# Kernel optimization log

Hardware: AMD Instinct MI355X
Metric: run time of the kernel (lower is better)

Reference implementation:

```python
import jax, jax.numpy as jnp
import numpy as np

LAMBDA_SOFTMAX = 9.0   # opt.lambda_softmax
LAMBDA_LSE = 6.0       # opt.lambda_lse
MARGIN = 0.2
EPS = 1e-8


def setup_inputs() -> dict:
    key = jax.random.key(0)
    k1, k2, k3, k4 = jax.random.split(key, 4)
    N, F, W, D = 64, 64, 40, 512
    images = jax.random.normal(k1, (N, F, D), dtype=jnp.float32)
    captions = jax.random.normal(k2, (N, W, D), dtype=jnp.float32)
    img_lens = jax.random.randint(k3, (N,), F // 2, F + 1)
    cap_lens = jax.random.randint(k4, (N,), W // 2, W + 1)
    return {"images": images, "captions": captions,
            "img_lens": img_lens, "cap_lens": cap_lens}


def _xattn_scores(images, captions, img_lens, cap_lens):
    # images: (N, F, D) queries; captions: (N, W, D) contexts
    N, F, D = images.shape
    W = captions.shape[1]
    fmask = jnp.arange(F)[None, :] < img_lens[:, None]   # (N_img, F)
    wmask = jnp.arange(W)[None, :] < cap_lens[:, None]   # (N_cap, W)
    # raw attention for every (caption j, image i) pair: (j, i, w, f)
    A = jnp.einsum('jwd,ifd->jiwf', captions, images)
    pair_mask = wmask[:, None, :, None] & fmask[None, :, None, :]
    A = jnp.where(pair_mask, A, 0.0)
    # clipped_l2norm: LeakyReLU(0.1) then l2-normalize along frame axis
    A = jnp.where(A > 0, A, 0.1 * A)
    A = A / (jnp.sqrt(jnp.sum(A * A, axis=3, keepdims=True)) + EPS)
    # softmax over words (sourceL) with temperature lambda_softmax
    logits = jnp.swapaxes(A, 2, 3) * LAMBDA_SOFTMAX       # (j, i, f, w)
    logits = jnp.where(wmask[:, None, None, :], logits, -jnp.inf)
    aw = jax.nn.softmax(logits, axis=-1)                  # (j, i, f, w)
    # weighted context per frame: (j, i, f, d)
    wctx = jnp.einsum('jifw,jwd->jifd', aw, captions)
    # per-frame cosine similarity between image frame and weighted context
    num = jnp.einsum('ifd,jifd->jif', images, wctx)
    n1 = jnp.linalg.norm(images, axis=-1)                 # (i, f)
    n2 = jnp.linalg.norm(wctx, axis=-1)                   # (j, i, f)
    sim = num / jnp.maximum(n1[None, :, :] * n2, EPS)     # (j, i, f)
    # LogSumExp aggregation over valid frames (unstabilized, as in torch)
    e = jnp.exp(sim * LAMBDA_LSE) * fmask[None, :, :]
    scores = jnp.log(jnp.sum(e, axis=-1)) / LAMBDA_LSE    # (n_cap, n_img)
    return scores


def reference(images, captions, img_lens, cap_lens):
    S = _xattn_scores(images, captions, img_lens, cap_lens)  # (N, N)
    diag = jnp.diagonal(S)
    eye = jnp.eye(S.shape[0], dtype=bool)
    cost_s = jnp.maximum(MARGIN + S - diag[:, None], 0.0)
    cost_im = jnp.maximum(MARGIN + S - diag[None, :], 0.0)
    cost_s = jnp.where(eye, 0.0, cost_s)
    cost_im = jnp.where(eye, 0.0, cost_im)
    # max_violation=True: hardest negative per row/col
    return jnp.max(cost_s, axis=1).sum() + jnp.max(cost_im, axis=0).sum()
```

## Files before the change

### kernel.cpp

```cpp
#include <hip/hip_runtime.h>
#include <math.h>

#define N 64
#define F 64
#define W 40
#define D 512
#define LSM 9.0f
#define LLSE 6.0f
#define MARG 0.2f
#define ESTR 56

typedef _Float16 f16x8 __attribute__((ext_vector_type(8)));
typedef _Float16 f16x4 __attribute__((ext_vector_type(4)));
typedef float f32x4 __attribute__((ext_vector_type(4)));

__device__ inline void gll16(const void* g, void* l) {
  __builtin_amdgcn_global_load_lds(
      (const __attribute__((address_space(1))) unsigned int*)g,
      (__attribute__((address_space(3))) unsigned int*)l, 16, 0, 0);
}


__global__ __launch_bounds__(512) void k_pre(
    const float* __restrict__ img, const float* __restrict__ cap,
    _Float16* __restrict__ img_h, _Float16* __restrict__ cap_h,
    _Float16* __restrict__ G_h, float* __restrict__ n1) {
  __shared__ __align__(16) _Float16 capT[4 * 48 * 128];
  int t = threadIdx.x;
  int b = blockIdx.x;
  if (b < 256) {
    int i = b >> 2;
    int f = ((b & 3) << 4) + (t >> 5);
    int q = t & 31;
    const float* row = img + ((size_t)i * F + f) * D + q * 16;
    _Float16* dsti = img_h + (size_t)i * 32768;
    int fsw = (f & 7) << 3;
    float s = 0.f;
    int d0 = q * 16;
    int ch = d0 >> 6, din = d0 & 63;
#pragma unroll
    for (int k = 0; k < 2; ++k) {
      float4 u = *(const float4*)(row + k * 8);
      float4 v = *(const float4*)(row + k * 8 + 4);
      s += u.x * u.x + u.y * u.y + u.z * u.z + u.w * u.w;
      s += v.x * v.x + v.y * v.y + v.z * v.z + v.w * v.w;
      f16x8 h;
      h[0] = (_Float16)u.x; h[1] = (_Float16)u.y; h[2] = (_Float16)u.z; h[3] = (_Float16)u.w;
      h[4] = (_Float16)v.x; h[5] = (_Float16)v.y; h[6] = (_Float16)v.z; h[7] = (_Float16)v.w;
      *(f16x8*)(dsti + ch * 4096 + f * 64 + ((din + k * 8) ^ fsw)) = h;
    }
    s += __shfl_xor(s, 1);
    s += __shfl_xor(s, 2);
    s += __shfl_xor(s, 4);
    s += __shfl_xor(s, 8);
    s += __shfl_xor(s, 16);
    if (q == 0) n1[i * F + f] = sqrtf(s);
  } else {
    int j = b - 256;
    int lane = t & 63, wv = t >> 6;
    const float* src = cap + (size_t)j * W * D;
    _Float16* dst = cap_h + (size_t)j * 24576;
#pragma unroll
    for (int k = 0; k < 6; ++k) {
      int slot = t + k * 512;
      int w = slot >> 6, d = (slot & 63) * 8;
      float4 u = {0.f, 0.f, 0.f, 0.f}, v = {0.f, 0.f, 0.f, 0.f};
      if (w < W) {
        u = *(const float4*)(src + (size_t)w * D + d);
        v = *(const float4*)(src + (size_t)w * D + d + 4);
      }
      f16x8 h;
      h[0] = (_Float16)u.x; h[1] = (_Float16)u.y; h[2] = (_Float16)u.z; h[3] = (_Float16)u.w;
      h[4] = (_Float16)v.x; h[5] = (_Float16)v.y; h[6] = (_Float16)v.z; h[7] = (_Float16)v.w;
      int wsw = (w & 7) << 3;
      int ch2 = d >> 6, din2 = d & 63;
      *(f16x8*)(dst + ch2 * 3072 + w * 64 + (din2 ^ wsw)) = h;
      int chO = d >> 7, dinO = d & 127;
      *(f16x8*)(capT + chO * 6144 + w * 128 + (dinO ^ wsw)) = h;
    }
    __syncthreads();
    int rlo = lane & 15, hi = lane >> 4;
    int koff = hi * 8, sw = (rlo & 7) << 3;
    _Float16* gb = G_h + (size_t)j * 3072;
    for (int tile = wv; tile < 9; tile += 8) {
      int mt = tile / 3, kt = tile % 3;
      f32x4 acc = (f32x4)0.f;
#pragma unroll
      for (int ks = 0; ks < 16; ++ks) {
        int kk = ks * 32 + koff;
        int ch = kk >> 7, din = (kk & 127) ^ sw;
        f16x8 af = *(const f16x8*)(capT + ch * 6144 + (mt * 16 + rlo) * 128 + din);
        f16x8 bf = *(const f16x8*)(capT + ch * 6144 + (kt * 16 + rlo) * 128 + din);
        acc = __builtin_amdgcn_mfma_f32_16x16x32_f16(af, bf, acc, 0, 0, 0);
      }
#pragma unroll
      for (int r = 0; r < 4; ++r) {
        int w = mt * 16 + hi * 4 + r, k = kt * 16 + rlo;
        float val = (w < W && k < W) ? acc[r] : 0.f;
        gb[w * 64 + k] = (_Float16)val;
      }
    }
    if (t < 96) {
      int w = t >> 1, c8 = 48 + (t & 1) * 8;
      *(f16x8*)(gb + w * 64 + c8) = (f16x8)(_Float16)0.f;
    }
  }
}

__global__ __launch_bounds__(512, 4) void k_main(
    const _Float16* __restrict__ img_h, const _Float16* __restrict__ cap_h,
    const int* __restrict__ imgL, const int* __restrict__ capL,
    const float* __restrict__ n1g, const _Float16* __restrict__ G_h,
    float* __restrict__ S) {
  __shared__ __align__(16) char buf[81920];

  int t = threadIdx.x;
  int lane = t & 63, wv = t >> 6;
  int rlo = lane & 15, hi = lane >> 4;
  int koff = hi * 8;
  int sw = (rlo & 7) << 3;

  int bid = blockIdx.x;
  int xcd = bid & 7, s0 = bid >> 3;
  int jloc = wv & 3, iloc = wv >> 2;
  int i = (xcd & 3) * 16 + (s0 & 7) * 2 + iloc;
  int j = (xcd >> 2) * 32 + (s0 >> 3) * 4 + jloc;

  int iL = imgL[i], cL = capL[j];

  const char* capb = (const char*)cap_h + (size_t)(j - jloc) * 49152;
  const char* imgb = (const char*)img_h + (size_t)(i - iloc) * 65536;

  const char* bsrc[5];
  int cstr[5], mdst[5];
#pragma unroll
  for (int s = 0; s < 5; ++s) {
    int m = s * 8 + wv;
    if (m < 24) {
      bsrc[s] = capb + (m / 6) * 49152 + (m % 6) * 1024 + lane * 16;
      cstr[s] = 6144;
    } else {
      int e = m - 24;
      bsrc[s] = imgb + (e >> 3) * 65536 + (e & 7) * 1024 + lane * 16;
      cstr[s] = 8192;
    }
    mdst[s] = m * 1024;
  }

  f32x4 acc[3][4];
#pragma unroll
  for (int mt = 0; mt < 3; ++mt)
#pragma unroll
    for (int nt = 0; nt < 4; ++nt) acc[mt][nt] = (f32x4)0.f;

#pragma unroll
  for (int s = 0; s < 5; ++s) gll16(bsrc[s], buf + mdst[s]);

#pragma unroll
  for (int c = 0; c < 8; ++c) {
    if (c < 7) {
      char* db = buf + ((c + 1) & 1) * 40960;
#pragma unroll
      for (int s = 0; s < 5; ++s) gll16(bsrc[s] + (c + 1) * cstr[s], db + mdst[s]);
      asm volatile("s_waitcnt vmcnt(5)" ::: "memory");
    } else {
      asm volatile("s_waitcnt vmcnt(0)" ::: "memory");
    }
    __builtin_amdgcn_s_barrier();
    __builtin_amdgcn_sched_barrier(0);
    const char* cb = buf + (c & 1) * 40960;
    const _Float16* myCap = (const _Float16*)cb + jloc * 3072;
    const _Float16* myImg = (const _Float16*)(cb + 24576) + iloc * 4096;
#pragma unroll
    for (int ks = 0; ks < 2; ++ks) {
      int col = (ks * 32 + koff) ^ sw;
      f16x8 af[3], bf[4];
#pragma unroll
      for (int mt = 0; mt < 3; ++mt) af[mt] = *(const f16x8*)(myCap + (mt * 16 + rlo) * 64 + col);
#pragma unroll
      for (int nt = 0; nt < 4; ++nt) bf[nt] = *(const f16x8*)(myImg + (nt * 16 + rlo) * 64 + col);
#pragma unroll
      for (int mt = 0; mt < 3; ++mt)
#pragma unroll
        for (int nt = 0; nt < 4; ++nt)
          acc[mt][nt] = __builtin_amdgcn_mfma_f32_16x16x32_f16(af[mt], bf[nt], acc[mt][nt], 0, 0, 0);
    }
    __builtin_amdgcn_sched_barrier(0);
    __builtin_amdgcn_s_barrier();
  }

  _Float16* Ew = (_Float16*)(buf + wv * 7168);
  float n1lane = n1g[i * F + lane];

  float rinv[3][4];
#pragma unroll
  for (int mt = 0; mt < 3; ++mt)
#pragma unroll
    for (int r = 0; r < 4; ++r) {
      float s = 0.f;
#pragma unroll
      for (int nt = 0; nt < 4; ++nt) {
        float a = acc[mt][nt][r];
        float l = a > 0.f ? a : 0.1f * a;
        s += ((nt * 16 + rlo) < iL) ? l * l : 0.f;
      }
#pragma unroll
      for (int d = 1; d < 16; d <<= 1) s += __shfl_xor(s, d);
      rinv[mt][r] = 1.f / (sqrtf(s) + 1e-8f);
    }

  float sn[4] = {0.f, 0.f, 0.f, 0.f};
#pragma unroll
  for (int mt = 0; mt < 3; ++mt)
#pragma unroll
    for (int nt = 0; nt < 4; ++nt) {
      f16x4 ev;
#pragma unroll
      for (int r = 0; r < 4; ++r) {
        int w = mt * 16 + hi * 4 + r;
        float a = acc[mt][nt][r];
        float l = a > 0.f ? a : 0.1f * a;
        float e = (w < cL) ? __expf(LSM * l * rinv[mt][r]) : 0.f;
        sn[nt] = fmaf(e, a, sn[nt]);
        ev[r] = (_Float16)e;
      }
      *(f16x4*)(Ew + (nt * 16 + rlo) * ESTR + mt * 16 + hi * 4) = ev;
    }
#pragma unroll
  for (int nt = 0; nt < 4; ++nt) {
    sn[nt] += __shfl_xor(sn[nt], 16);
    sn[nt] += __shfl_xor(sn[nt], 32);
  }

  const _Float16* gB = G_h + (size_t)j * 3072 + rlo * 64 + koff;
  f32x4 P[4][3];
#pragma unroll
  for (int mtl = 0; mtl < 4; ++mtl)
#pragma unroll
    for (int ntl = 0; ntl < 3; ++ntl) P[mtl][ntl] = (f32x4)0.f;
#pragma unroll
  for (int ks2 = 0; ks2 < 2; ++ks2) {
    int kk2 = ks2 * 32;
    f16x8 bfg[3];
#pragma unroll
    for (int ntl = 0; ntl < 3; ++ntl) bfg[ntl] = *(const f16x8*)(gB + ntl * 1024 + kk2);
#pragma unroll
    for (int mtl = 0; mtl < 4; ++mtl) {
      f16x8 af = *(const f16x8*)(Ew + (mtl * 16 + rlo) * ESTR + kk2 + koff);
#pragma unroll
      for (int ntl = 0; ntl < 3; ++ntl)
        P[mtl][ntl] = __builtin_amdgcn_mfma_f32_16x16x32_f16(af, bfg[ntl], P[mtl][ntl], 0, 0, 0);
    }
  }

  float ef = 0.f;
#pragma unroll
  for (int mtl = 0; mtl < 4; ++mtl) {
#pragma unroll
    for (int rr = 0; rr < 4; ++rr) {
      int fm = mtl * 16 + hi * 4 + rr;
      float n2s = 0.f;
#pragma unroll
      for (int ntl = 0; ntl < 3; ++ntl) {
        float evv = (float)Ew[fm * ESTR + ntl * 16 + rlo];
        n2s = fmaf(P[mtl][ntl][rr], evv, n2s);
      }
#pragma unroll
      for (int d = 1; d < 16; d <<= 1) n2s += __shfl_xor(n2s, d);
      float nm = __shfl(sn[mtl], hi * 4 + rr);
      float n1v = __shfl(n1lane, fm);
      float denom = n1v * sqrtf(fmaxf(n2s, 0.f));
      float sim = nm / fmaxf(denom, 1e-20f);
      ef += (fm < iL) ? __expf(LLSE * sim) : 0.f;
    }
  }
  ef += __shfl_xor(ef, 16);
  ef += __shfl_xor(ef, 32);
  if (lane == 0) S[(j << 6) + i] = __logf(ef) * (1.f / LLSE);
}

__global__ void k_loss(const float* __restrict__ S, float* __restrict__ out) {
  __shared__ float red[128];
  int t = threadIdx.x;
  float m = -1e30f;
  if (t < 64) {
    int a = t;
    float da = S[a * N + a];
    for (int b = 0; b < N; ++b)
      if (b != a) m = fmaxf(m, MARG + S[a * N + b] - da);
  } else {
    int b = t - 64;
    float db = S[b * N + b];
    for (int a = 0; a < N; ++a)
      if (a != b) m = fmaxf(m, MARG + S[a * N + b] - db);
  }
  red[t] = fmaxf(m, 0.f);
  __syncthreads();
  if (t < 64) {
    float v = red[t] + red[t + 64];
#pragma unroll
    for (int off = 1; off < 64; off <<= 1) v += __shfl_xor(v, off);
    if (t == 0) *out = v;
  }
}

extern "C" void kernel_launch(void* const* d_in, const int* in_sizes, int n_in,
                              void* d_out, int out_size, void* d_ws, size_t ws_size,
                              hipStream_t stream) {
  const float* img = (const float*)d_in[0];
  const float* cap = (const float*)d_in[1];
  const int* imgL = (const int*)d_in[2];
  const int* capL = (const int*)d_in[3];

  char* wsb = (char*)d_ws;
  float* n1 = (float*)wsb;
  float* S = (float*)(wsb + 16384);
  _Float16* img_h = (_Float16*)(wsb + 32768);
  _Float16* cap_h = (_Float16*)(wsb + 32768 + 4194304);
  _Float16* G_h = (_Float16*)(wsb + 32768 + 4194304 + 3145728);

  k_pre<<<320, 512, 0, stream>>>(img, cap, img_h, cap_h, G_h, n1);
  k_main<<<512, 512, 0, stream>>>(img_h, cap_h, imgL, capL, n1, G_h, S);
  k_loss<<<1, 128, 0, stream>>>(S, (float*)d_out);
}
```

Baseline: 56.74 us.

## Split fused attention kernel into GEMM kernel and separate epilogue kernel

The fused main kernel is split in two. k_gemm computes the raw caption-image attention tiles, applies the masks, and writes them to global memory as fp16. A new k_epi kernel, one 256-thread block per pair, reloads each tile and does the LeakyReLU norm, softmax, G-based context norm and LSE in shared memory. This is meant to ease register pressure and raise parallelism in the epilogue, at the cost of an extra kernel launch and a roughly 20 MB global round trip for the attention tiles.

```diff
diff --git a/kernel.cpp b/kernel.cpp
--- a/kernel.cpp
+++ b/kernel.cpp
@@ -8,7 +8,6 @@
 #define LSM 9.0f
 #define LLSE 6.0f
 #define MARG 0.2f
-#define ESTR 56
 
 typedef _Float16 f16x8 __attribute__((ext_vector_type(8)));
 typedef _Float16 f16x4 __attribute__((ext_vector_type(4)));
@@ -79,7 +78,8 @@
       *(f16x8*)(capT + chO * 6144 + w * 128 + (dinO ^ wsw)) = h;
     }
     __syncthreads();
-    int rlo = lane & 15, hi = lane >> 4;
+    int lane2 = t & 63;
+    int rlo = lane2 & 15, hi = lane2 >> 4;
     int koff = hi * 8, sw = (rlo & 7) << 3;
     _Float16* gb = G_h + (size_t)j * 3072;
     for (int tile = wv; tile < 9; tile += 8) {
@@ -107,11 +107,10 @@
   }
 }
 
-__global__ __launch_bounds__(512, 4) void k_main(
+__global__ __launch_bounds__(512, 4) void k_gemm(
     const _Float16* __restrict__ img_h, const _Float16* __restrict__ cap_h,
     const int* __restrict__ imgL, const int* __restrict__ capL,
-    const float* __restrict__ n1g, const _Float16* __restrict__ G_h,
-    float* __restrict__ S) {
+    _Float16* __restrict__ A_g) {
   __shared__ __align__(16) char buf[81920];
 
   int t = threadIdx.x;
@@ -189,94 +188,132 @@
     __builtin_amdgcn_s_barrier();
   }
 
-  _Float16* Ew = (_Float16*)(buf + wv * 7168);
-  float n1lane = n1g[i * F + lane];
-
-  float rinv[3][4];
+  _Float16* Ag = A_g + (size_t)((j << 6) + i) * 2560;
 #pragma unroll
   for (int mt = 0; mt < 3; ++mt)
 #pragma unroll
     for (int r = 0; r < 4; ++r) {
-      float s = 0.f;
-#pragma unroll
-      for (int nt = 0; nt < 4; ++nt) {
-        float a = acc[mt][nt][r];
+      int w = mt * 16 + hi * 4 + r;
+      if (w < W) {
+#pragma unroll
+        for (int nt = 0; nt < 4; ++nt) {
+          int f = nt * 16 + rlo;
+          float v = (w < cL && f < iL) ? acc[mt][nt][r] : 0.f;
+          Ag[w * 64 + f] = (_Float16)v;
+        }
+      }
+    }
+}
+
+__global__ __launch_bounds__(256, 8) void k_epi(
+    const _Float16* __restrict__ A_g, const _Float16* __restrict__ G_h,
+    const int* __restrict__ imgL, const int* __restrict__ capL,
+    const float* __restrict__ n1g, float* __restrict__ S) {
+  __shared__ __align__(16) _Float16 Al[40 * 72];
+  __shared__ __align__(16) _Float16 Es[64 * 72];
+  __shared__ float rinv_s[W];
+  __shared__ float numu[F];
+  __shared__ float red[4];
+
+  int t = threadIdx.x;
+  int lane = t & 63, wv = t >> 6;
+  int rlo = lane & 15, hi = lane >> 4;
+  int koff = hi * 8;
+
+  int bid = blockIdx.x;
+  int j = bid >> 6, i = bid & 63;
+  int iL = imgL[i], cL = capL[j];
+
+  for (int k = t; k < 576; k += 256) ((f16x8*)Es)[k] = (f16x8)(_Float16)0.f;
+
+  if (t < 160) {
+    const _Float16* src = A_g + (size_t)bid * 2560 + t * 16;
+    f16x8 a0 = *(const f16x8*)src;
+    f16x8 a1 = *(const f16x8*)(src + 8);
+    int row = t >> 2, colb = (t & 3) * 16;
+    *(f16x8*)(Al + row * 72 + colb) = a0;
+    *(f16x8*)(Al + row * 72 + colb + 8) = a1;
+  }
+  __syncthreads();
+
+  if (t < 160) {
+    int w = t >> 2, q = t & 3;
+    const _Float16* p = Al + w * 72 + q * 16;
+    float s = 0.f;
+#pragma unroll
+    for (int k = 0; k < 2; ++k) {
+      f16x8 h = *(const f16x8*)(p + k * 8);
+#pragma unroll
+      for (int e = 0; e < 8; ++e) {
+        float a = (float)h[e];
         float l = a > 0.f ? a : 0.1f * a;
-        s += ((nt * 16 + rlo) < iL) ? l * l : 0.f;
-      }
-#pragma unroll
-      for (int d = 1; d < 16; d <<= 1) s += __shfl_xor(s, d);
-      rinv[mt][r] = 1.f / (sqrtf(s) + 1e-8f);
-    }
-
-  float sn[4] = {0.f, 0.f, 0.f, 0.f};
-#pragma unroll
-  for (int mt = 0; mt < 3; ++mt)
-#pragma unroll
-    for (int nt = 0; nt < 4; ++nt) {
-      f16x4 ev;
-#pragma unroll
-      for (int r = 0; r < 4; ++r) {
-        int w = mt * 16 + hi * 4 + r;
-        float a = acc[mt][nt][r];
-        float l = a > 0.f ? a : 0.1f * a;
-        float e = (w < cL) ? __expf(LSM * l * rinv[mt][r]) : 0.f;
-        sn[nt] = fmaf(e, a, sn[nt]);
-        ev[r] = (_Float16)e;
-      }
-      *(f16x4*)(Ew + (nt * 16 + rlo) * ESTR + mt * 16 + hi * 4) = ev;
-    }
-#pragma unroll
-  for (int nt = 0; nt < 4; ++nt) {
-    sn[nt] += __shfl_xor(sn[nt], 16);
-    sn[nt] += __shfl_xor(sn[nt], 32);
-  }
-
-  const _Float16* gB = G_h + (size_t)j * 3072 + rlo * 64 + koff;
-  f32x4 P[4][3];
-#pragma unroll
-  for (int mtl = 0; mtl < 4; ++mtl)
-#pragma unroll
-    for (int ntl = 0; ntl < 3; ++ntl) P[mtl][ntl] = (f32x4)0.f;
+        s += l * l;
+      }
+    }
+    s += __shfl_xor(s, 1);
+    s += __shfl_xor(s, 2);
+    if (q == 0) rinv_s[w] = 1.f / (sqrtf(s) + 1e-8f);
+  }
+  __syncthreads();
+
+  {
+    int c = t & 3, f = t >> 2;
+    float sn = 0.f;
+#pragma unroll
+    for (int k = 0; k < 10; ++k) {
+      int w = c + 4 * k;
+      float a = (float)Al[w * 72 + f];
+      float l = a > 0.f ? a : 0.1f * a;
+      float e = (w < cL) ? __expf(LSM * l * rinv_s[w]) : 0.f;
+      sn = fmaf(e, a, sn);
+      Es[f * 72 + w] = (_Float16)e;
+    }
+    sn += __shfl_xor(sn, 1);
+    sn += __shfl_xor(sn, 2);
+    if (c == 0) numu[f] = sn;
+  }
+  __syncthreads();
+
+  int fr = wv * 16 + rlo;
+  const _Float16* gB = G_h + (size_t)j * 3072;
+  f32x4 P[3];
+#pragma unroll
+  for (int ntl = 0; ntl < 3; ++ntl) P[ntl] = (f32x4)0.f;
 #pragma unroll
   for (int ks2 = 0; ks2 < 2; ++ks2) {
-    int kk2 = ks2 * 32;
-    f16x8 bfg[3];
-#pragma unroll
-    for (int ntl = 0; ntl < 3; ++ntl) bfg[ntl] = *(const f16x8*)(gB + ntl * 1024 + kk2);
-#pragma unroll
-    for (int mtl = 0; mtl < 4; ++mtl) {
-      f16x8 af = *(const f16x8*)(Ew + (mtl * 16 + rlo) * ESTR + kk2 + koff);
-#pragma unroll
-      for (int ntl = 0; ntl < 3; ++ntl)
-        P[mtl][ntl] = __builtin_amdgcn_mfma_f32_16x16x32_f16(af, bfg[ntl], P[mtl][ntl], 0, 0, 0);
+    int kk = ks2 * 32 + koff;
+    f16x8 ea = *(const f16x8*)(Es + fr * 72 + kk);
+#pragma unroll
+    for (int ntl = 0; ntl < 3; ++ntl) {
+      f16x8 gb = *(const f16x8*)(gB + (ntl * 16 + rlo) * 64 + kk);
+      P[ntl] = __builtin_amdgcn_mfma_f32_16x16x32_f16(ea, gb, P[ntl], 0, 0, 0);
     }
   }
 
   float ef = 0.f;
 #pragma unroll
-  for (int mtl = 0; mtl < 4; ++mtl) {
-#pragma unroll
-    for (int rr = 0; rr < 4; ++rr) {
-      int fm = mtl * 16 + hi * 4 + rr;
-      float n2s = 0.f;
-#pragma unroll
-      for (int ntl = 0; ntl < 3; ++ntl) {
-        float evv = (float)Ew[fm * ESTR + ntl * 16 + rlo];
-        n2s = fmaf(P[mtl][ntl][rr], evv, n2s);
-      }
-#pragma unroll
-      for (int d = 1; d < 16; d <<= 1) n2s += __shfl_xor(n2s, d);
-      float nm = __shfl(sn[mtl], hi * 4 + rr);
-      float n1v = __shfl(n1lane, fm);
-      float denom = n1v * sqrtf(fmaxf(n2s, 0.f));
-      float sim = nm / fmaxf(denom, 1e-20f);
-      ef += (fm < iL) ? __expf(LLSE * sim) : 0.f;
-    }
-  }
-  ef += __shfl_xor(ef, 16);
-  ef += __shfl_xor(ef, 32);
-  if (lane == 0) S[(j << 6) + i] = __logf(ef) * (1.f / LLSE);
+  for (int rr = 0; rr < 4; ++rr) {
+    int fm = wv * 16 + hi * 4 + rr;
+    float n2s = 0.f;
+#pragma unroll
+    for (int ntl = 0; ntl < 3; ++ntl) {
+      float evv = (float)Es[fm * 72 + ntl * 16 + rlo];
+      n2s = fmaf(P[ntl][rr], evv, n2s);
+    }
+#pragma unroll
+    for (int d = 1; d < 16; d <<= 1) n2s += __shfl_xor(n2s, d);
+    float nm = numu[fm];
+    float n1v = n1g[i * F + fm];
+    float denom = n1v * sqrtf(fmaxf(n2s, 0.f));
+    float sim = nm / fmaxf(denom, 1e-20f);
+    ef += (fm < iL) ? __expf(LLSE * sim) : 0.f;
+  }
+  float val = (rlo == 0) ? ef : 0.f;
+#pragma unroll
+  for (int d = 1; d < 64; d <<= 1) val += __shfl_xor(val, d);
+  if (lane == 0) red[wv] = val;
+  __syncthreads();
+  if (t == 0) S[(j << 6) + i] = __logf(red[0] + red[1] + red[2] + red[3]) * (1.f / LLSE);
 }
 
 __global__ void k_loss(const float* __restrict__ S, float* __restrict__ out) {
@@ -318,8 +355,10 @@
   _Float16* img_h = (_Float16*)(wsb + 32768);
   _Float16* cap_h = (_Float16*)(wsb + 32768 + 4194304);
   _Float16* G_h = (_Float16*)(wsb + 32768 + 4194304 + 3145728);
+  _Float16* A_g = (_Float16*)(wsb + 32768 + 4194304 + 3145728 + 393216);
 
   k_pre<<<320, 512, 0, stream>>>(img, cap, img_h, cap_h, G_h, n1);
-  k_main<<<512, 512, 0, stream>>>(img_h, cap_h, imgL, capL, n1, G_h, S);
+  k_gemm<<<512, 512, 0, stream>>>(img_h, cap_h, imgL, capL, A_g);
+  k_epi<<<4096, 256, 0, stream>>>(A_g, G_h, imgL, capL, n1, S);
   k_loss<<<1, 128, 0, stream>>>(S, (float*)d_out);
 }
```

Measured after the change: 61.70 us. +8.8%, slower.

## Enlarge main-kernel block tile to 4 captions by 4 images with 2 pairs per wave

Applied to the files above, without the earlier changes.

The block tile grows from 4 captions x 2 images to 4 captions x 4 images, so the grid drops from 512 to 256 blocks and each fp16 chunk staged in LDS is reused by twice as many waves. Each wave now accumulates a 6x4 MFMA tile covering two caption-image pairs, then runs the softmax, context-norm and LSE epilogue twice in sequence. MFMA sections are wrapped in s_setprio to raise wave priority. The trade-off is a larger LDS buffer (112 KB), fewer resident blocks, more accumulator registers per wave and a longer serial epilogue per wave, which leaves less parallelism to hide latency.

```diff
diff --git a/kernel.cpp b/kernel.cpp
--- a/kernel.cpp
+++ b/kernel.cpp
@@ -79,7 +79,8 @@
       *(f16x8*)(capT + chO * 6144 + w * 128 + (dinO ^ wsw)) = h;
     }
     __syncthreads();
-    int rlo = lane & 15, hi = lane >> 4;
+    int lane2 = t & 63;
+    int rlo = lane2 & 15, hi = lane2 >> 4;
     int koff = hi * 8, sw = (rlo & 7) << 3;
     _Float16* gb = G_h + (size_t)j * 3072;
     for (int tile = wv; tile < 9; tile += 8) {
@@ -107,34 +108,37 @@
   }
 }
 
-__global__ __launch_bounds__(512, 4) void k_main(
+__global__ __launch_bounds__(512, 2) void k_fused(
     const _Float16* __restrict__ img_h, const _Float16* __restrict__ cap_h,
     const int* __restrict__ imgL, const int* __restrict__ capL,
     const float* __restrict__ n1g, const _Float16* __restrict__ G_h,
     float* __restrict__ S) {
-  __shared__ __align__(16) char buf[81920];
+  __shared__ __align__(16) char buf[114688];
 
   int t = threadIdx.x;
   int lane = t & 63, wv = t >> 6;
   int rlo = lane & 15, hi = lane >> 4;
   int koff = hi * 8;
   int sw = (rlo & 7) << 3;
+  int wm = wv >> 2, wn = wv & 3;
 
   int bid = blockIdx.x;
   int xcd = bid & 7, s0 = bid >> 3;
-  int jloc = wv & 3, iloc = wv >> 2;
-  int i = (xcd & 3) * 16 + (s0 & 7) * 2 + iloc;
-  int j = (xcd >> 2) * 32 + (s0 >> 3) * 4 + jloc;
-
-  int iL = imgL[i], cL = capL[j];
-
-  const char* capb = (const char*)cap_h + (size_t)(j - jloc) * 49152;
-  const char* imgb = (const char*)img_h + (size_t)(i - iloc) * 65536;
-
-  const char* bsrc[5];
-  int cstr[5], mdst[5];
-#pragma unroll
-  for (int s = 0; s < 5; ++s) {
+  int bj = (xcd & 3) * 4 + (s0 & 3);
+  int bi = (xcd >> 2) * 8 + (s0 >> 2);
+
+  int i = bi * 4 + wn;
+  int ja = bj * 4 + wm * 2;
+  int iL = imgL[i];
+  int cLa = capL[ja], cLb = capL[ja + 1];
+
+  const char* capb = (const char*)cap_h + (size_t)bj * 4 * 49152;
+  const char* imgb = (const char*)img_h + (size_t)bi * 4 * 65536;
+
+  const char* bsrc[7];
+  int cstr[7], mdst[7];
+#pragma unroll
+  for (int s = 0; s < 7; ++s) {
     int m = s * 8 + wv;
     if (m < 24) {
       bsrc[s] = capb + (m / 6) * 49152 + (m % 6) * 1024 + lane * 16;
@@ -147,43 +151,49 @@
     mdst[s] = m * 1024;
   }
 
-  f32x4 acc[3][4];
-#pragma unroll
-  for (int mt = 0; mt < 3; ++mt)
+  f32x4 acc[6][4];
+#pragma unroll
+  for (int mt = 0; mt < 6; ++mt)
 #pragma unroll
     for (int nt = 0; nt < 4; ++nt) acc[mt][nt] = (f32x4)0.f;
 
 #pragma unroll
-  for (int s = 0; s < 5; ++s) gll16(bsrc[s], buf + mdst[s]);
+  for (int s = 0; s < 7; ++s) gll16(bsrc[s], buf + mdst[s]);
 
 #pragma unroll
   for (int c = 0; c < 8; ++c) {
     if (c < 7) {
-      char* db = buf + ((c + 1) & 1) * 40960;
-#pragma unroll
-      for (int s = 0; s < 5; ++s) gll16(bsrc[s] + (c + 1) * cstr[s], db + mdst[s]);
-      asm volatile("s_waitcnt vmcnt(5)" ::: "memory");
+      char* db = buf + ((c + 1) & 1) * 57344;
+#pragma unroll
+      for (int s = 0; s < 7; ++s) gll16(bsrc[s] + (c + 1) * cstr[s], db + mdst[s]);
+      asm volatile("s_waitcnt vmcnt(7)" ::: "memory");
     } else {
       asm volatile("s_waitcnt vmcnt(0)" ::: "memory");
     }
     __builtin_amdgcn_s_barrier();
     __builtin_amdgcn_sched_barrier(0);
-    const char* cb = buf + (c & 1) * 40960;
-    const _Float16* myCap = (const _Float16*)cb + jloc * 3072;
-    const _Float16* myImg = (const _Float16*)(cb + 24576) + iloc * 4096;
+    const char* cb = buf + (c & 1) * 57344;
+    const _Float16* Al = (const _Float16*)cb;
+    const _Float16* Bl = (const _Float16*)(cb + 24576) + wn * 4096;
 #pragma unroll
     for (int ks = 0; ks < 2; ++ks) {
       int col = (ks * 32 + koff) ^ sw;
-      f16x8 af[3], bf[4];
-#pragma unroll
-      for (int mt = 0; mt < 3; ++mt) af[mt] = *(const f16x8*)(myCap + (mt * 16 + rlo) * 64 + col);
-#pragma unroll
-      for (int nt = 0; nt < 4; ++nt) bf[nt] = *(const f16x8*)(myImg + (nt * 16 + rlo) * 64 + col);
-#pragma unroll
-      for (int mt = 0; mt < 3; ++mt)
+      f16x8 bf[4], af[6];
+#pragma unroll
+      for (int nt = 0; nt < 4; ++nt) bf[nt] = *(const f16x8*)(Bl + (nt * 16 + rlo) * 64 + col);
+#pragma unroll
+      for (int mt = 0; mt < 6; ++mt) {
+        int blk = wm * 2 + (mt >= 3 ? 1 : 0);
+        int w = (mt >= 3 ? mt - 3 : mt) * 16 + rlo;
+        af[mt] = *(const f16x8*)(Al + blk * 3072 + w * 64 + col);
+      }
+      __builtin_amdgcn_s_setprio(1);
+#pragma unroll
+      for (int mt = 0; mt < 6; ++mt)
 #pragma unroll
         for (int nt = 0; nt < 4; ++nt)
           acc[mt][nt] = __builtin_amdgcn_mfma_f32_16x16x32_f16(af[mt], bf[nt], acc[mt][nt], 0, 0, 0);
+      __builtin_amdgcn_s_setprio(0);
     }
     __builtin_amdgcn_sched_barrier(0);
     __builtin_amdgcn_s_barrier();
@@ -192,91 +202,98 @@
   _Float16* Ew = (_Float16*)(buf + wv * 7168);
   float n1lane = n1g[i * F + lane];
 
-  float rinv[3][4];
-#pragma unroll
-  for (int mt = 0; mt < 3; ++mt)
-#pragma unroll
-    for (int r = 0; r < 4; ++r) {
-      float s = 0.f;
+#pragma unroll
+  for (int p = 0; p < 2; ++p) {
+    int j = ja + p;
+    int cL = p ? cLb : cLa;
+    int mb = p * 3;
+
+    float rinv[3][4];
+#pragma unroll
+    for (int mt = 0; mt < 3; ++mt)
+#pragma unroll
+      for (int r = 0; r < 4; ++r) {
+        float s = 0.f;
+#pragma unroll
+        for (int nt = 0; nt < 4; ++nt) {
+          float a = acc[mb + mt][nt][r];
+          float l = a > 0.f ? a : 0.1f * a;
+          s += ((nt * 16 + rlo) < iL) ? l * l : 0.f;
+        }
+#pragma unroll
+        for (int d = 1; d < 16; d <<= 1) s += __shfl_xor(s, d);
+        rinv[mt][r] = 1.f / (sqrtf(s) + 1e-8f);
+      }
+
+    float sn[4] = {0.f, 0.f, 0.f, 0.f};
+#pragma unroll
+    for (int mt = 0; mt < 3; ++mt)
 #pragma unroll
       for (int nt = 0; nt < 4; ++nt) {
-        float a = acc[mt][nt][r];
-        float l = a > 0.f ? a : 0.1f * a;
-        s += ((nt * 16 + rlo) < iL) ? l * l : 0.f;
-      }
-#pragma unroll
-      for (int d = 1; d < 16; d <<= 1) s += __shfl_xor(s, d);
-      rinv[mt][r] = 1.f / (sqrtf(s) + 1e-8f);
-    }
-
-  float sn[4] = {0.f, 0.f, 0.f, 0.f};
-#pragma unroll
-  for (int mt = 0; mt < 3; ++mt)
+        f16x4 ev;
+#pragma unroll
+        for (int r = 0; r < 4; ++r) {
+          int w = mt * 16 + hi * 4 + r;
+          float a = acc[mb + mt][nt][r];
+          float l = a > 0.f ? a : 0.1f * a;
+          float e = (w < cL) ? __expf(LSM * l * rinv[mt][r]) : 0.f;
+          sn[nt] = fmaf(e, a, sn[nt]);
+          ev[r] = (_Float16)e;
+        }
+        *(f16x4*)(Ew + (nt * 16 + rlo) * ESTR + mt * 16 + hi * 4) = ev;
+      }
 #pragma unroll
     for (int nt = 0; nt < 4; ++nt) {
-      f16x4 ev;
-#pragma unroll
-      for (int r = 0; r < 4; ++r) {
-        int w = mt * 16 + hi * 4 + r;
-        float a = acc[mt][nt][r];
-        float l = a > 0.f ? a : 0.1f * a;
-        float e = (w < cL) ? __expf(LSM * l * rinv[mt][r]) : 0.f;
-        sn[nt] = fmaf(e, a, sn[nt]);
-        ev[r] = (_Float16)e;
-      }
-      *(f16x4*)(Ew + (nt * 16 + rlo) * ESTR + mt * 16 + hi * 4) = ev;
-    }
-#pragma unroll
-  for (int nt = 0; nt < 4; ++nt) {
-    sn[nt] += __shfl_xor(sn[nt], 16);
-    sn[nt] += __shfl_xor(sn[nt], 32);
-  }
-
-  const _Float16* gB = G_h + (size_t)j * 3072 + rlo * 64 + koff;
-  f32x4 P[4][3];
-#pragma unroll
-  for (int mtl = 0; mtl < 4; ++mtl)
-#pragma unroll
-    for (int ntl = 0; ntl < 3; ++ntl) P[mtl][ntl] = (f32x4)0.f;
-#pragma unroll
-  for (int ks2 = 0; ks2 < 2; ++ks2) {
-    int kk2 = ks2 * 32;
-    f16x8 bfg[3];
-#pragma unroll
-    for (int ntl = 0; ntl < 3; ++ntl) bfg[ntl] = *(const f16x8*)(gB + ntl * 1024 + kk2);
+      sn[nt] += __shfl_xor(sn[nt], 16);
+      sn[nt] += __shfl_xor(sn[nt], 32);
+    }
+
+    const _Float16* gB = G_h + (size_t)j * 3072 + rlo * 64 + koff;
+    f32x4 P[4][3];
+#pragma unroll
+    for (int mtl = 0; mtl < 4; ++mtl)
+#pragma unroll
+      for (int ntl = 0; ntl < 3; ++ntl) P[mtl][ntl] = (f32x4)0.f;
+#pragma unroll
+    for (int ks2 = 0; ks2 < 2; ++ks2) {
+      int kk2 = ks2 * 32;
+      f16x8 bfg[3];
+#pragma unroll
+      for (int ntl = 0; ntl < 3; ++ntl) bfg[ntl] = *(const f16x8*)(gB + ntl * 1024 + kk2);
+#pragma unroll
+      for (int mtl = 0; mtl < 4; ++mtl) {
+        f16x8 af = *(const f16x8*)(Ew + (mtl * 16 + rlo) * ESTR + kk2 + koff);
+#pragma unroll
+        for (int ntl = 0; ntl < 3; ++ntl)
+          P[mtl][ntl] = __builtin_amdgcn_mfma_f32_16x16x32_f16(af, bfg[ntl], P[mtl][ntl], 0, 0, 0);
+      }
+    }
+
+    float ef = 0.f;
 #pragma unroll
     for (int mtl = 0; mtl < 4; ++mtl) {
-      f16x8 af = *(const f16x8*)(Ew + (mtl * 16 + rlo) * ESTR + kk2 + koff);
-#pragma unroll
-      for (int ntl = 0; ntl < 3; ++ntl)
-        P[mtl][ntl] = __builtin_amdgcn_mfma_f32_16x16x32_f16(af, bfg[ntl], P[mtl][ntl], 0, 0, 0);
-    }
-  }
-
-  float ef = 0.f;
-#pragma unroll
-  for (int mtl = 0; mtl < 4; ++mtl) {
-#pragma unroll
-    for (int rr = 0; rr < 4; ++rr) {
-      int fm = mtl * 16 + hi * 4 + rr;
-      float n2s = 0.f;
-#pragma unroll
-      for (int ntl = 0; ntl < 3; ++ntl) {
-        float evv = (float)Ew[fm * ESTR + ntl * 16 + rlo];
-        n2s = fmaf(P[mtl][ntl][rr], evv, n2s);
-      }
-#pragma unroll
-      for (int d = 1; d < 16; d <<= 1) n2s += __shfl_xor(n2s, d);
-      float nm = __shfl(sn[mtl], hi * 4 + rr);
-      float n1v = __shfl(n1lane, fm);
-      float denom = n1v * sqrtf(fmaxf(n2s, 0.f));
-      float sim = nm / fmaxf(denom, 1e-20f);
-      ef += (fm < iL) ? __expf(LLSE * sim) : 0.f;
-    }
-  }
-  ef += __shfl_xor(ef, 16);
-  ef += __shfl_xor(ef, 32);
-  if (lane == 0) S[(j << 6) + i] = __logf(ef) * (1.f / LLSE);
+#pragma unroll
+      for (int rr = 0; rr < 4; ++rr) {
+        int fm = mtl * 16 + hi * 4 + rr;
+        float n2s = 0.f;
+#pragma unroll
+        for (int ntl = 0; ntl < 3; ++ntl) {
+          float evv = (float)Ew[fm * ESTR + ntl * 16 + rlo];
+          n2s = fmaf(P[mtl][ntl][rr], evv, n2s);
+        }
+#pragma unroll
+        for (int d = 1; d < 16; d <<= 1) n2s += __shfl_xor(n2s, d);
+        float nm = __shfl(sn[mtl], hi * 4 + rr);
+        float n1v = __shfl(n1lane, fm);
+        float denom = n1v * sqrtf(fmaxf(n2s, 0.f));
+        float sim = nm / fmaxf(denom, 1e-20f);
+        ef += (fm < iL) ? __expf(LLSE * sim) : 0.f;
+      }
+    }
+    ef += __shfl_xor(ef, 16);
+    ef += __shfl_xor(ef, 32);
+    if (lane == 0) S[(j << 6) + i] = __logf(ef) * (1.f / LLSE);
+  }
 }
 
 __global__ void k_loss(const float* __restrict__ S, float* __restrict__ out) {
@@ -320,6 +337,6 @@
   _Float16* G_h = (_Float16*)(wsb + 32768 + 4194304 + 3145728);
 
   k_pre<<<320, 512, 0, stream>>>(img, cap, img_h, cap_h, G_h, n1);
-  k_main<<<512, 512, 0, stream>>>(img_h, cap_h, imgL, capL, n1, G_h, S);
+  k_fused<<<256, 512, 0, stream>>>(img_h, cap_h, imgL, capL, n1, G_h, S);
   k_loss<<<1, 128, 0, stream>>>(S, (float*)d_out);
 }
```

New measurement: 54.07 us. 4.7% less time.
